# Optimization experiments

Hardware: AMD Instinct MI355X
Metric: run time of the kernel (lower is better)

Reference implementation:

```python
import jax, jax.numpy as jnp
import numpy as np

HEADS = 8

def setup_inputs() -> dict:
    key = jax.random.key(0)
    k1, k2 = jax.random.split(key)
    f_s = jax.random.normal(k1, (8, 256, 32, 32), dtype=jnp.float32)
    f_t = jax.random.normal(k2, (8, 256, 32, 32), dtype=jnp.float32)
    return {"f_s": f_s, "f_t": f_t}

def _to_tokens(x, heads):
    # 'b (h d) x y -> b h (x y) d'
    b, c, h, w = x.shape
    d = c // heads
    return x.reshape(b, heads, d, h * w).transpose(0, 1, 3, 2)

def reference(f_s, f_t):
    b, c, h, w = f_s.shape
    q = _to_tokens(f_s, HEADS)   # [b, H, n, d]
    k = _to_tokens(f_t, HEADS)
    v = _to_tokens(f_s, HEADS)
    # unscaled QK^T softmax V (faithful to source: no 1/sqrt(d) scaling)
    sim = jnp.einsum('bhid,bhjd->bhij', q, k)          # [b, H, n, n]
    attn = jax.nn.softmax(sim, axis=-1)
    out = jnp.einsum('bhij,bhjd->bhid', attn, v)       # [b, H, n, d]
    # 'b h (x y) d -> b (h d) x y'
    out = out.transpose(0, 1, 3, 2).reshape(b, c, h, w)
    loss = jnp.mean((out - f_t) ** 2)
    return loss
```

## Files before the change

### kernel.cpp

```cpp
#include <hip/hip_runtime.h>
#include <hip/hip_bf16.h>


typedef __attribute__((ext_vector_type(4))) float f32x4;
typedef __attribute__((ext_vector_type(8))) short bf16x8;
typedef __attribute__((ext_vector_type(4))) unsigned u32x4;

#define KOFF 0
#define VOFF 65536

__device__ __forceinline__ unsigned cvtpk(float a, float b) {
    unsigned r;
    asm("v_cvt_pk_bf16_f32 %0, %1, %2" : "=v"(r) : "v"(a), "v"(b));
    return r;
}
#define SWAP32(a, b) asm("v_permlane32_swap_b32 %0, %1" : "+v"(a), "+v"(b))
#define SWAP16(a, b) asm("v_permlane16_swap_b32 %0, %1" : "+v"(a), "+v"(b))

__device__ __forceinline__ float exp2fast(float x) {
#if __has_builtin(__builtin_amdgcn_exp2f)
    return __builtin_amdgcn_exp2f(x);
#else
    return exp2f(x);
#endif
}

__global__ __launch_bounds__(512, 2)
void attn_mse_kernel(const float* __restrict__ fs, const float* __restrict__ ft,
                     float* __restrict__ out)
{
    __shared__ __align__(16) unsigned char smem[131072];

    const int tid  = threadIdx.x;
    const int lane = tid & 63;
    const int w    = tid >> 6;
    const int g    = lane >> 4;
    const int c    = lane & 15;

    const int bid  = blockIdx.x;
    const int pair = (bid & 7) * 8 + ((bid >> 3) & 7);
    const int q0   = (bid >> 6) * 256;

    const float* qb = fs + (size_t)pair * 32768;
    const float* kb = ft + (size_t)pair * 32768;

    const int p_ = c >> 2, jq = c & 3;
    const int dp = 4 * p_ + g;
    const int w0 = p_ * 64 + 16 * jq + 4 * (0 ^ p_) + g;
    const int w1 = p_ * 64 + 16 * jq + 4 * (1 ^ p_) + g;
    const int w2 = p_ * 64 + 16 * jq + 4 * (2 ^ p_) + g;
    const int w3 = p_ * 64 + 16 * jq + 4 * (3 ^ p_) + g;

    {
        const float sc = 1.44269504f;
        #pragma unroll
        for (int st = 0; st < 2; ++st) {
            const float* r0 = qb + (size_t)(2 * dp) * 1024 + (q0 + w * 32 + st * 16) + 4 * jq;
            const float4 a = *(const float4*)(r0);
            const float4 b = *(const float4*)(r0 + 1024);
            unsigned* dst = (unsigned*)(smem + VOFF + w * 2048 + st * 1024);
            dst[w0] = cvtpk(a.x * sc, b.x * sc);
            dst[w1] = cvtpk(a.y * sc, b.y * sc);
            dst[w2] = cvtpk(a.z * sc, b.z * sc);
            dst[w3] = cvtpk(a.w * sc, b.w * sc);
        }
    }
    const bf16x8 qf0 = *(const bf16x8*)(smem + VOFF + w * 2048 + ((lane ^ g) << 4));
    const bf16x8 qf1 = *(const bf16x8*)(smem + VOFF + w * 2048 + 1024 + ((lane ^ g) << 4));
    __syncthreads();

    #pragma unroll
    for (int st = 0; st < 8; ++st) {
        const float* r0 = kb + (size_t)(2 * dp) * 1024 + (w * 128 + st * 16) + 4 * jq;
        const float4 a = *(const float4*)(r0);
        const float4 b = *(const float4*)(r0 + 1024);
        unsigned* dst = (unsigned*)(smem + KOFF + (w * 8 + st) * 1024);
        dst[w0] = cvtpk(a.x, b.x);
        dst[w1] = cvtpk(a.y, b.y);
        dst[w2] = cvtpk(a.z, b.z);
        dst[w3] = cvtpk(a.w, b.w);
    }
    {
        const int dv = w * 4 + g;
        #pragma unroll
        for (int tt = 0; tt < 16; ++tt) {
            const float4 vv = *(const float4*)(qb + (size_t)dv * 1024 + tt * 64 + 4 * c);
            const unsigned lo = cvtpk(vv.x, vv.y), hi = cvtpk(vv.z, vv.w);
            *(unsigned long long*)(smem + VOFF + tt * 4096 + dv * 128 +
                                   ((8 * c) ^ ((dv & 7) << 4))) =
                (unsigned long long)lo | ((unsigned long long)hi << 32);
        }
    }
    __syncthreads();

    f32x4 O[2][2];
    #pragma unroll
    for (int a = 0; a < 2; ++a)
        #pragma unroll
        for (int b = 0; b < 2; ++b)
            O[a][b] = f32x4{0.f, 0.f, 0.f, 0.f};
    float l0 = 0.f, l1 = 0.f;

    for (int t = 0; t < 16; ++t) {
        const int tabs = (t + 2 * w) & 15;
        const unsigned char* bK = smem + KOFF + tabs * 4096;
        const unsigned char* bV = smem + VOFF + tabs * 4096;

        bf16x8 kf[4], vb[2][2];
        #pragma unroll
        for (int Mt = 0; Mt < 4; ++Mt)
            kf[Mt] = *(const bf16x8*)(bK + Mt * 1024 + ((lane ^ g) << 4));
        #pragma unroll
        for (int ks = 0; ks < 2; ++ks)
            #pragma unroll
            for (int df = 0; df < 2; ++df)
                vb[ks][df] = *(const bf16x8*)(bV + (c + 16 * df) * 128 +
                               (((unsigned)(ks * 64 + g * 16)) ^ ((c & 7) << 4)));

        f32x4 S[4][2];
        __builtin_amdgcn_s_setprio(1);
        #pragma unroll
        for (int Mt = 0; Mt < 4; ++Mt) {
            const f32x4 z = {0.f, 0.f, 0.f, 0.f};
            S[Mt][0] = __builtin_amdgcn_mfma_f32_16x16x32_bf16(kf[Mt], qf0, z, 0, 0, 0);
            S[Mt][1] = __builtin_amdgcn_mfma_f32_16x16x32_bf16(kf[Mt], qf1, z, 0, 0, 0);
        }
        __builtin_amdgcn_s_setprio(0);

        float ps0 = 0.f, ps1 = 0.f;
        #pragma unroll
        for (int Mt = 0; Mt < 4; ++Mt)
            #pragma unroll
            for (int r = 0; r < 4; ++r) {
                const float pv0 = exp2fast(S[Mt][0][r]);
                const float pv1 = exp2fast(S[Mt][1][r]);
                S[Mt][0][r] = pv0; ps0 += pv0;
                S[Mt][1][r] = pv1; ps1 += pv1;
            }
        l0 += ps0; l1 += ps1;

        #pragma unroll
        for (int is = 0; is < 2; ++is) {
            #pragma unroll
            for (int ks = 0; ks < 2; ++ks) {
                unsigned u0 = cvtpk(S[2 * ks][is][0],     S[2 * ks][is][1]);
                unsigned u1 = cvtpk(S[2 * ks][is][2],     S[2 * ks][is][3]);
                unsigned u2 = cvtpk(S[2 * ks + 1][is][0], S[2 * ks + 1][is][1]);
                unsigned u3 = cvtpk(S[2 * ks + 1][is][2], S[2 * ks + 1][is][3]);
                SWAP32(u0, u2); SWAP32(u1, u3);
                SWAP16(u0, u2); SWAP16(u1, u3);
                const u32x4 pw = {u0, u1, u2, u3};
                const bf16x8 pa = __builtin_bit_cast(bf16x8, pw);
                __builtin_amdgcn_s_setprio(1);
                O[is][0] = __builtin_amdgcn_mfma_f32_16x16x32_bf16(pa, vb[ks][0], O[is][0], 0, 0, 0);
                O[is][1] = __builtin_amdgcn_mfma_f32_16x16x32_bf16(pa, vb[ks][1], O[is][1], 0, 0, 0);
                __builtin_amdgcn_s_setprio(0);
            }
        }
    }

    l0 += __shfl_xor(l0, 16); l0 += __shfl_xor(l0, 32);
    l1 += __shfl_xor(l1, 16); l1 += __shfl_xor(l1, 32);
    const float li0 = 1.0f / l0;
    const float li1 = 1.0f / l1;

    float acc = 0.f;
    const int n0 = q0 + w * 32;
    #pragma unroll
    for (int is = 0; is < 2; ++is) {
        const float liv = is ? li1 : li0;
        #pragma unroll
        for (int r = 0; r < 4; ++r) {
            const float lr = __shfl(liv, g * 4 + r);
            const int n = n0 + is * 16 + g * 4 + r;
            #pragma unroll
            for (int Nd = 0; Nd < 2; ++Nd) {
                const int d = Nd * 16 + c;
                const float oo = O[is][Nd][r] * lr;
                const float tv = kb[(size_t)d * 1024 + n];
                const float e = oo - tv;
                acc += e * e;
            }
        }
    }
    #pragma unroll
    for (int off = 1; off < 64; off <<= 1) acc += __shfl_xor(acc, off);
    __syncthreads();
    float* lred = (float*)(smem);
    if (lane == 0) lred[w] = acc;
    __syncthreads();
    if (tid == 0) {
        float s = 0.f;
        #pragma unroll
        for (int i = 0; i < 8; ++i) s += lred[i];
        atomicAdd(out, s * (1.0f / 2097152.0f));
    }
}

extern "C" void kernel_launch(void* const* d_in, const int* in_sizes, int n_in,
                              void* d_out, int out_size, void* d_ws, size_t ws_size,
                              hipStream_t stream) {
    const float* fs = (const float*)d_in[0];
    const float* ft = (const float*)d_in[1];
    float* out = (float*)d_out;
    hipMemsetAsync(out, 0, sizeof(float), stream);
    attn_mse_kernel<<<dim3(256), dim3(512), 0, stream>>>(fs, ft, out);
}
```

Baseline: 28.02 us.

## Double-buffer LDS fragment loads and coalesce epilogue target reads via LDS

```diff
diff --git a/kernel.cpp b/kernel.cpp
--- a/kernel.cpp
+++ b/kernel.cpp
@@ -8,6 +8,7 @@
 
 #define KOFF 0
 #define VOFF 65536
+#define RED  130048
 
 __device__ __forceinline__ unsigned cvtpk(float a, float b) {
     unsigned r;
@@ -101,12 +102,12 @@
             O[a][b] = f32x4{0.f, 0.f, 0.f, 0.f};
     float l0 = 0.f, l1 = 0.f;
 
-    for (int t = 0; t < 16; ++t) {
+    bf16x8 kfA[4], kfB[4], vbA[2][2], vbB[2][2];
+
+    auto LDTILE = [&](int t, bf16x8* kf, bf16x8 (*vb)[2]) {
         const int tabs = (t + 2 * w) & 15;
         const unsigned char* bK = smem + KOFF + tabs * 4096;
         const unsigned char* bV = smem + VOFF + tabs * 4096;
-
-        bf16x8 kf[4], vb[2][2];
         #pragma unroll
         for (int Mt = 0; Mt < 4; ++Mt)
             kf[Mt] = *(const bf16x8*)(bK + Mt * 1024 + ((lane ^ g) << 4));
@@ -116,7 +117,9 @@
             for (int df = 0; df < 2; ++df)
                 vb[ks][df] = *(const bf16x8*)(bV + (c + 16 * df) * 128 +
                                (((unsigned)(ks * 64 + g * 16)) ^ ((c & 7) << 4)));
-
+    };
+
+    auto TILE = [&](const bf16x8* kf, const bf16x8 (*vb)[2]) {
         f32x4 S[4][2];
         __builtin_amdgcn_s_setprio(1);
         #pragma unroll
@@ -127,17 +130,21 @@
         }
         __builtin_amdgcn_s_setprio(0);
 
-        float ps0 = 0.f, ps1 = 0.f;
+        float pm[4][2];
         #pragma unroll
         for (int Mt = 0; Mt < 4; ++Mt)
             #pragma unroll
-            for (int r = 0; r < 4; ++r) {
-                const float pv0 = exp2fast(S[Mt][0][r]);
-                const float pv1 = exp2fast(S[Mt][1][r]);
-                S[Mt][0][r] = pv0; ps0 += pv0;
-                S[Mt][1][r] = pv1; ps1 += pv1;
+            for (int is = 0; is < 2; ++is) {
+                f32x4 p;
+                p[0] = exp2fast(S[Mt][is][0]);
+                p[1] = exp2fast(S[Mt][is][1]);
+                p[2] = exp2fast(S[Mt][is][2]);
+                p[3] = exp2fast(S[Mt][is][3]);
+                S[Mt][is] = p;
+                pm[Mt][is] = (p[0] + p[1]) + (p[2] + p[3]);
             }
-        l0 += ps0; l1 += ps1;
+        l0 += (pm[0][0] + pm[1][0]) + (pm[2][0] + pm[3][0]);
+        l1 += (pm[0][1] + pm[1][1]) + (pm[2][1] + pm[3][1]);
 
         #pragma unroll
         for (int is = 0; is < 2; ++is) {
@@ -157,6 +164,15 @@
                 __builtin_amdgcn_s_setprio(0);
             }
         }
+    };
+
+    LDTILE(0, kfA, vbA);
+    #pragma unroll 1
+    for (int t = 0; t < 16; t += 2) {
+        LDTILE(t + 1, kfB, vbB);
+        TILE(kfA, vbA);
+        if (t + 2 < 16) LDTILE(t + 2, kfA, vbA);
+        TILE(kfB, vbB);
     }
 
     l0 += __shfl_xor(l0, 16); l0 += __shfl_xor(l0, 32);
@@ -164,29 +180,33 @@
     const float li0 = 1.0f / l0;
     const float li1 = 1.0f / l1;
 
-    float acc = 0.f;
-    const int n0 = q0 + w * 32;
+    __syncthreads();
+    float* lw = (float*)smem + w * 1088;
     #pragma unroll
     for (int is = 0; is < 2; ++is) {
         const float liv = is ? li1 : li0;
         #pragma unroll
         for (int r = 0; r < 4; ++r) {
             const float lr = __shfl(liv, g * 4 + r);
-            const int n = n0 + is * 16 + g * 4 + r;
-            #pragma unroll
-            for (int Nd = 0; Nd < 2; ++Nd) {
-                const int d = Nd * 16 + c;
-                const float oo = O[is][Nd][r] * lr;
-                const float tv = kb[(size_t)d * 1024 + n];
-                const float e = oo - tv;
-                acc += e * e;
-            }
-        }
-    }
+            const int i = is * 16 + 4 * g + r;
+            lw[i * 34 + c]      = O[is][0][r] * lr;
+            lw[i * 34 + 16 + c] = O[is][1][r] * lr;
+        }
+    }
+    const int nl = lane & 31, hi = lane >> 5;
+    const float* tvb = kb + (size_t)(q0 + w * 32) + nl;
+    float a0 = 0.f, a1 = 0.f;
+    #pragma unroll
+    for (int s = 0; s < 8; ++s) {
+        const int d0 = 4 * s + hi, d1 = 4 * s + 2 + hi;
+        const float e0 = lw[nl * 34 + d0] - tvb[(size_t)d0 * 1024];
+        const float e1 = lw[nl * 34 + d1] - tvb[(size_t)d1 * 1024];
+        a0 += e0 * e0; a1 += e1 * e1;
+    }
+    float acc = a0 + a1;
     #pragma unroll
     for (int off = 1; off < 64; off <<= 1) acc += __shfl_xor(acc, off);
-    __syncthreads();
-    float* lred = (float*)(smem);
+    float* lred = (float*)(smem + RED);
     if (lane == 0) lred[w] = acc;
     __syncthreads();
     if (tid == 0) {
```

New measurement: 28.86 us. 3.0% more time.

## Split key range across two wave groups per block and merge partial outputs

Applied to the files above, without the earlier changes.

```diff
diff --git a/kernel.cpp b/kernel.cpp
--- a/kernel.cpp
+++ b/kernel.cpp
@@ -8,6 +8,9 @@
 
 #define KOFF 0
 #define VOFF 65536
+#define QOFF 131072
+#define LEX  34816
+#define REDX 35840
 
 __device__ __forceinline__ unsigned cvtpk(float a, float b) {
     unsigned r;
@@ -25,15 +28,17 @@
 #endif
 }
 
-__global__ __launch_bounds__(512, 2)
+__global__ __launch_bounds__(1024, 4)
 void attn_mse_kernel(const float* __restrict__ fs, const float* __restrict__ ft,
                      float* __restrict__ out)
 {
-    __shared__ __align__(16) unsigned char smem[131072];
+    __shared__ __align__(16) unsigned char smem[147456];
 
     const int tid  = threadIdx.x;
     const int lane = tid & 63;
     const int w    = tid >> 6;
+    const int wl   = w & 7;
+    const int jh   = w >> 3;
     const int g    = lane >> 4;
     const int c    = lane & 15;
 
@@ -51,47 +56,49 @@
     const int w2 = p_ * 64 + 16 * jq + 4 * (2 ^ p_) + g;
     const int w3 = p_ * 64 + 16 * jq + 4 * (3 ^ p_) + g;
 
+    #pragma unroll
+    for (int st = 0; st < 4; ++st) {
+        const int sub = w * 4 + st;
+        const float* r0 = kb + (size_t)(2 * dp) * 1024 + sub * 16 + 4 * jq;
+        const float4 a = *(const float4*)(r0);
+        const float4 b = *(const float4*)(r0 + 1024);
+        unsigned* dst = (unsigned*)(smem + KOFF + sub * 1024);
+        dst[w0] = cvtpk(a.x, b.x);
+        dst[w1] = cvtpk(a.y, b.y);
+        dst[w2] = cvtpk(a.z, b.z);
+        dst[w3] = cvtpk(a.w, b.w);
+    }
     {
+        const int dv  = lane >> 1;
+        const int j0v = (lane & 1) * 32;
+        #pragma unroll
+        for (int k2 = 0; k2 < 8; ++k2) {
+            const int jj = j0v + 4 * k2;
+            const float4 vv = *(const float4*)(qb + (size_t)dv * 1024 + w * 64 + jj);
+            const unsigned lo = cvtpk(vv.x, vv.y), hi = cvtpk(vv.z, vv.w);
+            *(unsigned long long*)(smem + VOFF + w * 4096 + dv * 128 +
+                                   ((2 * jj) ^ ((dv & 7) << 4))) =
+                (unsigned long long)lo | ((unsigned long long)hi << 32);
+        }
+    }
+    if (w < 8) {
         const float sc = 1.44269504f;
         #pragma unroll
         for (int st = 0; st < 2; ++st) {
             const float* r0 = qb + (size_t)(2 * dp) * 1024 + (q0 + w * 32 + st * 16) + 4 * jq;
             const float4 a = *(const float4*)(r0);
             const float4 b = *(const float4*)(r0 + 1024);
-            unsigned* dst = (unsigned*)(smem + VOFF + w * 2048 + st * 1024);
+            unsigned* dst = (unsigned*)(smem + QOFF + w * 2048 + st * 1024);
             dst[w0] = cvtpk(a.x * sc, b.x * sc);
             dst[w1] = cvtpk(a.y * sc, b.y * sc);
             dst[w2] = cvtpk(a.z * sc, b.z * sc);
             dst[w3] = cvtpk(a.w * sc, b.w * sc);
         }
     }
-    const bf16x8 qf0 = *(const bf16x8*)(smem + VOFF + w * 2048 + ((lane ^ g) << 4));
-    const bf16x8 qf1 = *(const bf16x8*)(smem + VOFF + w * 2048 + 1024 + ((lane ^ g) << 4));
-    __syncthreads();
-
-    #pragma unroll
-    for (int st = 0; st < 8; ++st) {
-        const float* r0 = kb + (size_t)(2 * dp) * 1024 + (w * 128 + st * 16) + 4 * jq;
-        const float4 a = *(const float4*)(r0);
-        const float4 b = *(const float4*)(r0 + 1024);
-        unsigned* dst = (unsigned*)(smem + KOFF + (w * 8 + st) * 1024);
-        dst[w0] = cvtpk(a.x, b.x);
-        dst[w1] = cvtpk(a.y, b.y);
-        dst[w2] = cvtpk(a.z, b.z);
-        dst[w3] = cvtpk(a.w, b.w);
-    }
-    {
-        const int dv = w * 4 + g;
-        #pragma unroll
-        for (int tt = 0; tt < 16; ++tt) {
-            const float4 vv = *(const float4*)(qb + (size_t)dv * 1024 + tt * 64 + 4 * c);
-            const unsigned lo = cvtpk(vv.x, vv.y), hi = cvtpk(vv.z, vv.w);
-            *(unsigned long long*)(smem + VOFF + tt * 4096 + dv * 128 +
-                                   ((8 * c) ^ ((dv & 7) << 4))) =
-                (unsigned long long)lo | ((unsigned long long)hi << 32);
-        }
-    }
-    __syncthreads();
+    __syncthreads();
+
+    const bf16x8 qf0 = *(const bf16x8*)(smem + QOFF + wl * 2048 + ((lane ^ g) << 4));
+    const bf16x8 qf1 = *(const bf16x8*)(smem + QOFF + wl * 2048 + 1024 + ((lane ^ g) << 4));
 
     f32x4 O[2][2];
     #pragma unroll
@@ -101,10 +108,11 @@
             O[a][b] = f32x4{0.f, 0.f, 0.f, 0.f};
     float l0 = 0.f, l1 = 0.f;
 
-    for (int t = 0; t < 16; ++t) {
-        const int tabs = (t + 2 * w) & 15;
-        const unsigned char* bK = smem + KOFF + tabs * 4096;
-        const unsigned char* bV = smem + VOFF + tabs * 4096;
+    #pragma unroll 1
+    for (int t = 0; t < 8; ++t) {
+        const int tile = jh * 8 + ((t + wl) & 7);
+        const unsigned char* bK = smem + KOFF + tile * 4096;
+        const unsigned char* bV = smem + VOFF + tile * 4096;
 
         bf16x8 kf[4], vb[2][2];
         #pragma unroll
@@ -117,36 +125,38 @@
                 vb[ks][df] = *(const bf16x8*)(bV + (c + 16 * df) * 128 +
                                (((unsigned)(ks * 64 + g * 16)) ^ ((c & 7) << 4)));
 
-        f32x4 S[4][2];
-        __builtin_amdgcn_s_setprio(1);
-        #pragma unroll
-        for (int Mt = 0; Mt < 4; ++Mt) {
-            const f32x4 z = {0.f, 0.f, 0.f, 0.f};
-            S[Mt][0] = __builtin_amdgcn_mfma_f32_16x16x32_bf16(kf[Mt], qf0, z, 0, 0, 0);
-            S[Mt][1] = __builtin_amdgcn_mfma_f32_16x16x32_bf16(kf[Mt], qf1, z, 0, 0, 0);
-        }
-        __builtin_amdgcn_s_setprio(0);
-
-        float ps0 = 0.f, ps1 = 0.f;
-        #pragma unroll
-        for (int Mt = 0; Mt < 4; ++Mt)
-            #pragma unroll
-            for (int r = 0; r < 4; ++r) {
-                const float pv0 = exp2fast(S[Mt][0][r]);
-                const float pv1 = exp2fast(S[Mt][1][r]);
-                S[Mt][0][r] = pv0; ps0 += pv0;
-                S[Mt][1][r] = pv1; ps1 += pv1;
-            }
-        l0 += ps0; l1 += ps1;
-
         #pragma unroll
         for (int is = 0; is < 2; ++is) {
+            const bf16x8 qf = is ? qf1 : qf0;
+            f32x4 S[4];
+            __builtin_amdgcn_s_setprio(1);
+            #pragma unroll
+            for (int Mt = 0; Mt < 4; ++Mt) {
+                const f32x4 z = {0.f, 0.f, 0.f, 0.f};
+                S[Mt] = __builtin_amdgcn_mfma_f32_16x16x32_bf16(kf[Mt], qf, z, 0, 0, 0);
+            }
+            __builtin_amdgcn_s_setprio(0);
+
+            float pm[4];
+            #pragma unroll
+            for (int Mt = 0; Mt < 4; ++Mt) {
+                f32x4 p;
+                p[0] = exp2fast(S[Mt][0]);
+                p[1] = exp2fast(S[Mt][1]);
+                p[2] = exp2fast(S[Mt][2]);
+                p[3] = exp2fast(S[Mt][3]);
+                S[Mt] = p;
+                pm[Mt] = (p[0] + p[1]) + (p[2] + p[3]);
+            }
+            const float ps = (pm[0] + pm[1]) + (pm[2] + pm[3]);
+            if (is == 0) l0 += ps; else l1 += ps;
+
             #pragma unroll
             for (int ks = 0; ks < 2; ++ks) {
-                unsigned u0 = cvtpk(S[2 * ks][is][0],     S[2 * ks][is][1]);
-                unsigned u1 = cvtpk(S[2 * ks][is][2],     S[2 * ks][is][3]);
-                unsigned u2 = cvtpk(S[2 * ks + 1][is][0], S[2 * ks + 1][is][1]);
-                unsigned u3 = cvtpk(S[2 * ks + 1][is][2], S[2 * ks + 1][is][3]);
+                unsigned u0 = cvtpk(S[2 * ks][0],     S[2 * ks][1]);
+                unsigned u1 = cvtpk(S[2 * ks][2],     S[2 * ks][3]);
+                unsigned u2 = cvtpk(S[2 * ks + 1][0], S[2 * ks + 1][1]);
+                unsigned u3 = cvtpk(S[2 * ks + 1][2], S[2 * ks + 1][3]);
                 SWAP32(u0, u2); SWAP32(u1, u3);
                 SWAP16(u0, u2); SWAP16(u1, u3);
                 const u32x4 pw = {u0, u1, u2, u3};
@@ -161,35 +171,72 @@
 
     l0 += __shfl_xor(l0, 16); l0 += __shfl_xor(l0, 32);
     l1 += __shfl_xor(l1, 16); l1 += __shfl_xor(l1, 32);
-    const float li0 = 1.0f / l0;
-    const float li1 = 1.0f / l1;
+
+    __syncthreads();
+    float* lex = (float*)(smem + LEX);
+    if (w >= 8) {
+        float* oh = (float*)(smem + (size_t)(w - 8) * 4352);
+        #pragma unroll
+        for (int is = 0; is < 2; ++is)
+            #pragma unroll
+            for (int r = 0; r < 4; ++r) {
+                const int row = is * 16 + 4 * g + r;
+                oh[row * 34 + c]      = O[is][0][r];
+                oh[row * 34 + 16 + c] = O[is][1][r];
+            }
+        if (g == 0) {
+            lex[(w - 8) * 32 + c]      = l0;
+            lex[(w - 8) * 32 + 16 + c] = l1;
+        }
+    }
+    __syncthreads();
 
     float acc = 0.f;
-    const int n0 = q0 + w * 32;
-    #pragma unroll
-    for (int is = 0; is < 2; ++is) {
-        const float liv = is ? li1 : li0;
-        #pragma unroll
-        for (int r = 0; r < 4; ++r) {
-            const float lr = __shfl(liv, g * 4 + r);
-            const int n = n0 + is * 16 + g * 4 + r;
-            #pragma unroll
-            for (int Nd = 0; Nd < 2; ++Nd) {
-                const int d = Nd * 16 + c;
-                const float oo = O[is][Nd][r] * lr;
-                const float tv = kb[(size_t)d * 1024 + n];
-                const float e = oo - tv;
-                acc += e * e;
-            }
-        }
-    }
-    #pragma unroll
-    for (int off = 1; off < 64; off <<= 1) acc += __shfl_xor(acc, off);
-    __syncthreads();
-    float* lred = (float*)(smem);
-    if (lane == 0) lred[w] = acc;
+    if (w < 8) {
+        const float* oh = (const float*)(smem + (size_t)w * 4352);
+        #pragma unroll
+        for (int is = 0; is < 2; ++is)
+            #pragma unroll
+            for (int r = 0; r < 4; ++r) {
+                const int row = is * 16 + 4 * g + r;
+                O[is][0][r] += oh[row * 34 + c];
+                O[is][1][r] += oh[row * 34 + 16 + c];
+            }
+        l0 += lex[w * 32 + c];
+        l1 += lex[w * 32 + 16 + c];
+        const float li0 = 1.0f / l0;
+        const float li1 = 1.0f / l1;
+
+        float* lw = (float*)(smem + VOFF) + w * 1088;
+        #pragma unroll
+        for (int is = 0; is < 2; ++is) {
+            const float liv = is ? li1 : li0;
+            #pragma unroll
+            for (int r = 0; r < 4; ++r) {
+                const float lr = __shfl(liv, g * 4 + r);
+                const int i = is * 16 + 4 * g + r;
+                lw[i * 34 + c]      = O[is][0][r] * lr;
+                lw[i * 34 + 16 + c] = O[is][1][r] * lr;
+            }
+        }
+        const int nl = lane & 31, h2 = lane >> 5;
+        const float* tvb = kb + (size_t)(q0 + w * 32) + nl;
+        float a0 = 0.f, a1 = 0.f;
+        #pragma unroll
+        for (int s = 0; s < 8; ++s) {
+            const int d0 = 4 * s + h2, d1 = 4 * s + 2 + h2;
+            const float e0 = lw[nl * 34 + d0] - tvb[(size_t)d0 * 1024];
+            const float e1 = lw[nl * 34 + d1] - tvb[(size_t)d1 * 1024];
+            a0 += e0 * e0; a1 += e1 * e1;
+        }
+        acc = a0 + a1;
+        #pragma unroll
+        for (int off = 1; off < 64; off <<= 1) acc += __shfl_xor(acc, off);
+        if (lane == 0) ((float*)(smem + REDX))[w] = acc;
+    }
     __syncthreads();
     if (tid == 0) {
+        const float* lred = (const float*)(smem + REDX);
         float s = 0.f;
         #pragma unroll
         for (int i = 0; i < 8; ++i) s += lred[i];
@@ -204,5 +251,5 @@
     const float* ft = (const float*)d_in[1];
     float* out = (float*)d_out;
     hipMemsetAsync(out, 0, sizeof(float), stream);
-    attn_mse_kernel<<<dim3(256), dim3(512), 0, stream>>>(fs, ft, out);
-}
+    attn_mse_kernel<<<dim3(256), dim3(1024), 0, stream>>>(fs, ft, out);
+}
```

New measurement: 30.51 us. 8.9% more time.

## Switch attention MFMAs from 16x16x32 to 32x32x16 tiles with LDS-staged epilogue

Applied to the files above, without the earlier changes.

```diff
diff --git a/kernel.cpp b/kernel.cpp
--- a/kernel.cpp
+++ b/kernel.cpp
@@ -3,11 +3,14 @@
 
 
 typedef __attribute__((ext_vector_type(4))) float f32x4;
+typedef __attribute__((ext_vector_type(16))) float f32x16;
 typedef __attribute__((ext_vector_type(8))) short bf16x8;
 typedef __attribute__((ext_vector_type(4))) unsigned u32x4;
 
 #define KOFF 0
 #define VOFF 65536
+#define QOFF 131072
+#define REDX 40960
 
 __device__ __forceinline__ unsigned cvtpk(float a, float b) {
     unsigned r;
@@ -15,27 +18,26 @@
     return r;
 }
 #define SWAP32(a, b) asm("v_permlane32_swap_b32 %0, %1" : "+v"(a), "+v"(b))
-#define SWAP16(a, b) asm("v_permlane16_swap_b32 %0, %1" : "+v"(a), "+v"(b))
 
-__device__ __forceinline__ float exp2fast(float x) {
-#if __has_builtin(__builtin_amdgcn_exp2f)
-    return __builtin_amdgcn_exp2f(x);
-#else
-    return exp2f(x);
-#endif
+__device__ __forceinline__ float expv(float x) {
+    float r;
+    asm("v_exp_f32 %0, %1" : "=v"(r) : "v"(x));
+    return r;
 }
 
 __global__ __launch_bounds__(512, 2)
 void attn_mse_kernel(const float* __restrict__ fs, const float* __restrict__ ft,
                      float* __restrict__ out)
 {
-    __shared__ __align__(16) unsigned char smem[131072];
+    __shared__ __align__(16) unsigned char smem[147456];
 
     const int tid  = threadIdx.x;
     const int lane = tid & 63;
     const int w    = tid >> 6;
     const int g    = lane >> 4;
     const int c    = lane & 15;
+    const int il   = lane & 31;
+    const int hi   = lane >> 5;
 
     const int bid  = blockIdx.x;
     const int pair = (bid & 7) * 8 + ((bid >> 3) & 7);
@@ -58,16 +60,17 @@
             const float* r0 = qb + (size_t)(2 * dp) * 1024 + (q0 + w * 32 + st * 16) + 4 * jq;
             const float4 a = *(const float4*)(r0);
             const float4 b = *(const float4*)(r0 + 1024);
-            unsigned* dst = (unsigned*)(smem + VOFF + w * 2048 + st * 1024);
+            unsigned* dst = (unsigned*)(smem + QOFF + w * 2048 + st * 1024);
             dst[w0] = cvtpk(a.x * sc, b.x * sc);
             dst[w1] = cvtpk(a.y * sc, b.y * sc);
             dst[w2] = cvtpk(a.z * sc, b.z * sc);
             dst[w3] = cvtpk(a.w * sc, b.w * sc);
         }
     }
-    const bf16x8 qf0 = *(const bf16x8*)(smem + VOFF + w * 2048 + ((lane ^ g) << 4));
-    const bf16x8 qf1 = *(const bf16x8*)(smem + VOFF + w * 2048 + 1024 + ((lane ^ g) << 4));
-    __syncthreads();
+    const unsigned qsel = ((unsigned)(il >> 4) << 10) | (((unsigned)(il >> 2) & 3) << 6);
+    const unsigned char* qbase = smem + QOFF + w * 2048 + qsel;
+    const bf16x8 qfa = *(const bf16x8*)(qbase + ((hi << 8) | (((il & 3) ^ hi) << 4)));
+    const bf16x8 qfb = *(const bf16x8*)(qbase + (((2 + hi) << 8) | (((il & 3) ^ (2 + hi)) << 4)));
 
     #pragma unroll
     for (int st = 0; st < 8; ++st) {
@@ -85,111 +88,88 @@
         #pragma unroll
         for (int tt = 0; tt < 16; ++tt) {
             const float4 vv = *(const float4*)(qb + (size_t)dv * 1024 + tt * 64 + 4 * c);
-            const unsigned lo = cvtpk(vv.x, vv.y), hi = cvtpk(vv.z, vv.w);
+            const unsigned lo = cvtpk(vv.x, vv.y), hh = cvtpk(vv.z, vv.w);
             *(unsigned long long*)(smem + VOFF + tt * 4096 + dv * 128 +
                                    ((8 * c) ^ ((dv & 7) << 4))) =
-                (unsigned long long)lo | ((unsigned long long)hi << 32);
+                (unsigned long long)lo | ((unsigned long long)hh << 32);
         }
     }
     __syncthreads();
 
-    f32x4 O[2][2];
+    f32x16 O, z16;
     #pragma unroll
-    for (int a = 0; a < 2; ++a)
-        #pragma unroll
-        for (int b = 0; b < 2; ++b)
-            O[a][b] = f32x4{0.f, 0.f, 0.f, 0.f};
-    float l0 = 0.f, l1 = 0.f;
+    for (int r = 0; r < 16; ++r) { O[r] = 0.f; z16[r] = 0.f; }
+    float lden = 0.f;
 
+    #pragma unroll 1
     for (int t = 0; t < 16; ++t) {
-        const int tabs = (t + 2 * w) & 15;
-        const unsigned char* bK = smem + KOFF + tabs * 4096;
-        const unsigned char* bV = smem + VOFF + tabs * 4096;
-
-        bf16x8 kf[4], vb[2][2];
-        #pragma unroll
-        for (int Mt = 0; Mt < 4; ++Mt)
-            kf[Mt] = *(const bf16x8*)(bK + Mt * 1024 + ((lane ^ g) << 4));
-        #pragma unroll
-        for (int ks = 0; ks < 2; ++ks)
-            #pragma unroll
-            for (int df = 0; df < 2; ++df)
-                vb[ks][df] = *(const bf16x8*)(bV + (c + 16 * df) * 128 +
-                               (((unsigned)(ks * 64 + g * 16)) ^ ((c & 7) << 4)));
-
-        f32x4 S[4][2];
-        __builtin_amdgcn_s_setprio(1);
-        #pragma unroll
-        for (int Mt = 0; Mt < 4; ++Mt) {
-            const f32x4 z = {0.f, 0.f, 0.f, 0.f};
-            S[Mt][0] = __builtin_amdgcn_mfma_f32_16x16x32_bf16(kf[Mt], qf0, z, 0, 0, 0);
-            S[Mt][1] = __builtin_amdgcn_mfma_f32_16x16x32_bf16(kf[Mt], qf1, z, 0, 0, 0);
-        }
-        __builtin_amdgcn_s_setprio(0);
-
-        float ps0 = 0.f, ps1 = 0.f;
-        #pragma unroll
-        for (int Mt = 0; Mt < 4; ++Mt)
-            #pragma unroll
-            for (int r = 0; r < 4; ++r) {
-                const float pv0 = exp2fast(S[Mt][0][r]);
-                const float pv1 = exp2fast(S[Mt][1][r]);
-                S[Mt][0][r] = pv0; ps0 += pv0;
-                S[Mt][1][r] = pv1; ps1 += pv1;
-            }
-        l0 += ps0; l1 += ps1;
+        const int tile = (t + 2 * w) & 15;
+        const unsigned char* vbase = smem + VOFF + tile * 4096 + il * 128;
 
         #pragma unroll
-        for (int is = 0; is < 2; ++is) {
+        for (int half = 0; half < 2; ++half) {
+            const unsigned char* kbs = smem + KOFF + (tile * 2 + half) * 2048 + qsel;
+            const bf16x8 ka0 = *(const bf16x8*)(kbs + ((hi << 8) | (((il & 3) ^ hi) << 4)));
+            const bf16x8 ka1 = *(const bf16x8*)(kbs + (((2 + hi) << 8) | (((il & 3) ^ (2 + hi)) << 4)));
+            f32x16 S;
+            __builtin_amdgcn_s_setprio(1);
+            S = __builtin_amdgcn_mfma_f32_32x32x16_bf16(ka0, qfa, z16, 0, 0, 0);
+            S = __builtin_amdgcn_mfma_f32_32x32x16_bf16(ka1, qfb, S, 0, 0, 0);
+            __builtin_amdgcn_s_setprio(0);
+
+            #pragma unroll
+            for (int r = 0; r < 16; ++r) S[r] = expv(S[r]);
+            const float t0 = (S[0] + S[1]) + (S[2] + S[3]);
+            const float t1 = (S[4] + S[5]) + (S[6] + S[7]);
+            const float t2 = (S[8] + S[9]) + (S[10] + S[11]);
+            const float t3 = (S[12] + S[13]) + (S[14] + S[15]);
+            lden += (t0 + t1) + (t2 + t3);
+
             #pragma unroll
             for (int ks = 0; ks < 2; ++ks) {
-                unsigned u0 = cvtpk(S[2 * ks][is][0],     S[2 * ks][is][1]);
-                unsigned u1 = cvtpk(S[2 * ks][is][2],     S[2 * ks][is][3]);
-                unsigned u2 = cvtpk(S[2 * ks + 1][is][0], S[2 * ks + 1][is][1]);
-                unsigned u3 = cvtpk(S[2 * ks + 1][is][2], S[2 * ks + 1][is][3]);
+                unsigned u0 = cvtpk(S[8 * ks + 0], S[8 * ks + 1]);
+                unsigned u1 = cvtpk(S[8 * ks + 2], S[8 * ks + 3]);
+                unsigned u2 = cvtpk(S[8 * ks + 4], S[8 * ks + 5]);
+                unsigned u3 = cvtpk(S[8 * ks + 6], S[8 * ks + 7]);
                 SWAP32(u0, u2); SWAP32(u1, u3);
-                SWAP16(u0, u2); SWAP16(u1, u3);
                 const u32x4 pw = {u0, u1, u2, u3};
                 const bf16x8 pa = __builtin_bit_cast(bf16x8, pw);
+                const unsigned col =
+                    ((unsigned)(2 * (half * 32 + ks * 16 + 8 * hi))) ^ ((il & 7) << 4);
+                const bf16x8 vbf = *(const bf16x8*)(vbase + col);
                 __builtin_amdgcn_s_setprio(1);
-                O[is][0] = __builtin_amdgcn_mfma_f32_16x16x32_bf16(pa, vb[ks][0], O[is][0], 0, 0, 0);
-                O[is][1] = __builtin_amdgcn_mfma_f32_16x16x32_bf16(pa, vb[ks][1], O[is][1], 0, 0, 0);
+                O = __builtin_amdgcn_mfma_f32_32x32x16_bf16(pa, vbf, O, 0, 0, 0);
                 __builtin_amdgcn_s_setprio(0);
             }
         }
     }
 
-    l0 += __shfl_xor(l0, 16); l0 += __shfl_xor(l0, 32);
-    l1 += __shfl_xor(l1, 16); l1 += __shfl_xor(l1, 32);
-    const float li0 = 1.0f / l0;
-    const float li1 = 1.0f / l1;
+    lden += __shfl_xor(lden, 32);
+    const float li = 1.0f / lden;
 
-    float acc = 0.f;
-    const int n0 = q0 + w * 32;
+    __syncthreads();
+    float* ow = (float*)smem + w * 1104;
     #pragma unroll
-    for (int is = 0; is < 2; ++is) {
-        const float liv = is ? li1 : li0;
-        #pragma unroll
-        for (int r = 0; r < 4; ++r) {
-            const float lr = __shfl(liv, g * 4 + r);
-            const int n = n0 + is * 16 + g * 4 + r;
-            #pragma unroll
-            for (int Nd = 0; Nd < 2; ++Nd) {
-                const int d = Nd * 16 + c;
-                const float oo = O[is][Nd][r] * lr;
-                const float tv = kb[(size_t)d * 1024 + n];
-                const float e = oo - tv;
-                acc += e * e;
-            }
-        }
+    for (int r = 0; r < 16; ++r) {
+        const int ir = (r & 3) + 8 * (r >> 2) + 4 * hi;
+        ow[ir * 33 + il] = O[r];
     }
+    const float* tvb = kb + (size_t)(q0 + w * 32) + il;
+    float a0 = 0.f, a1 = 0.f;
+    #pragma unroll
+    for (int s = 0; s < 8; ++s) {
+        const int d0 = 4 * s + hi, d1 = 4 * s + 2 + hi;
+        const float e0 = ow[il * 33 + d0] * li - tvb[(size_t)d0 * 1024];
+        const float e1 = ow[il * 33 + d1] * li - tvb[(size_t)d1 * 1024];
+        a0 += e0 * e0; a1 += e1 * e1;
+    }
+    float acc = a0 + a1;
     #pragma unroll
     for (int off = 1; off < 64; off <<= 1) acc += __shfl_xor(acc, off);
-    __syncthreads();
-    float* lred = (float*)(smem);
-    if (lane == 0) lred[w] = acc;
+    if (lane == 0) ((float*)(smem + REDX))[w] = acc;
     __syncthreads();
     if (tid == 0) {
+        const float* lred = (const float*)(smem + REDX);
         float s = 0.f;
         #pragma unroll
         for (int i = 0; i < 8; ++i) s += lred[i];
```

After: 27.50 us. About the same (-1.9%).
